# Kernel tuning notes

Measured on AMD Instinct MI355X. Metric: run time of the kernel, lower is better.

Reference implementation:

```python
import jax, jax.numpy as jnp
import numpy as np

B, M, L, D = 4, 128, 512, 768
NEG = -1e30


def setup_inputs() -> dict:
    key = jax.random.key(0)
    k1, k2 = jax.random.split(key)
    h = jax.random.normal(k1, (B, L, D), dtype=jnp.float32)
    mention_masks = jax.random.randint(k2, (B, M, L), 0, 2, dtype=jnp.int32)
    return {"h": h, "mention_masks": mention_masks}


def reference(h, mention_masks):
    # h: [B, L, D]; mention_masks: [B, M, L] (0/1)
    # Faithful to: m = (mask == 0).float() * -1e30; (m + h).max(dim=2)
    m = (mention_masks == 0).astype(h.dtype) * NEG          # [B, M, L]
    # broadcast add then max over token dim L -> [B, M, D]
    mention_reprs = jnp.max(h[:, None, :, :] + m[:, :, :, None], axis=2)
    return mention_reprs
```

## Files before the change

### kernel.cpp

```cpp
#include <hip/hip_runtime.h>

#define BB 4
#define MM 128
#define LL 512
#define DD 768
#define NEGF (-1e30f)

struct F3 { float x, y, z; };

__global__ __launch_bounds__(512, 2) void mention_max_kernel(
    const float* __restrict__ h, const int* __restrict__ mask,
    float* __restrict__ out)
{
    const int lane = threadIdx.x & 63;
    const int wave = threadIdx.x >> 6;
    const int dch  = blockIdx.x;
    const int mch  = blockIdx.y;
    const int b    = blockIdx.z;

    const int d0 = dch * 192 + lane * 3;
    const int m0 = mch * 8;
    const int l0 = wave * 64;

    const int* mp = mask + ((size_t)(b * MM + m0)) * LL + l0 + lane;
    int mv[8];
#pragma unroll
    for (int m = 0; m < 8; ++m) mv[m] = mp[m * LL];

    const F3* hp = (const F3*)(h + ((size_t)(b * LL + l0)) * DD + d0);
    F3 r0[32];
#pragma unroll
    for (int i = 0; i < 32; ++i) r0[i] = hp[(size_t)i * (DD / 3)];

    unsigned lobits[8], hibits[8];
#pragma unroll
    for (int m = 0; m < 8; ++m) {
        unsigned long long bl = __ballot(mv[m] != 0);
        lobits[m] = (unsigned)bl;
        hibits[m] = (unsigned)(bl >> 32);
    }

    F3 r1[32];
#pragma unroll
    for (int i = 0; i < 32; ++i) r1[i] = hp[(size_t)(i + 32) * (DD / 3)];

    F3 acc[8];
#pragma unroll
    for (int m = 0; m < 8; ++m) { acc[m].x = NEGF; acc[m].y = NEGF; acc[m].z = NEGF; }

#pragma unroll
    for (int m = 0; m < 8; ++m) {
        const unsigned w32 = lobits[m];
        F3 a = acc[m];
#pragma unroll
        for (int i = 0; i < 32; i += 2) {
            const float ad0 = ((w32 >> i) & 1u) ? 0.0f : NEGF;
            const float ad1 = ((w32 >> (i + 1)) & 1u) ? 0.0f : NEGF;
            a.x = fmaxf(fmaxf(r0[i].x + ad0, r0[i + 1].x + ad1), a.x);
            a.y = fmaxf(fmaxf(r0[i].y + ad0, r0[i + 1].y + ad1), a.y);
            a.z = fmaxf(fmaxf(r0[i].z + ad0, r0[i + 1].z + ad1), a.z);
        }
        acc[m] = a;
    }
#pragma unroll
    for (int m = 0; m < 8; ++m) {
        const unsigned w32 = hibits[m];
        F3 a = acc[m];
#pragma unroll
        for (int i = 0; i < 32; i += 2) {
            const float ad0 = ((w32 >> i) & 1u) ? 0.0f : NEGF;
            const float ad1 = ((w32 >> (i + 1)) & 1u) ? 0.0f : NEGF;
            a.x = fmaxf(fmaxf(r1[i].x + ad0, r1[i + 1].x + ad1), a.x);
            a.y = fmaxf(fmaxf(r1[i].y + ad0, r1[i + 1].y + ad1), a.y);
            a.z = fmaxf(fmaxf(r1[i].z + ad0, r1[i + 1].z + ad1), a.z);
        }
        acc[m] = a;
    }

    __shared__ float red[8][8][3][64];
#pragma unroll
    for (int m = 0; m < 8; ++m) {
        red[wave][m][0][lane] = acc[m].x;
        red[wave][m][1][lane] = acc[m].y;
        red[wave][m][2][lane] = acc[m].z;
    }
    __syncthreads();

    {
        const int m  = (int)(threadIdx.x >> 6);
        const int ln = (int)(threadIdx.x & 63);
        float vx = red[0][m][0][ln];
        float vy = red[0][m][1][ln];
        float vz = red[0][m][2][ln];
#pragma unroll
        for (int w = 1; w < 8; ++w) {
            vx = fmaxf(vx, red[w][m][0][ln]);
            vy = fmaxf(vy, red[w][m][1][ln]);
            vz = fmaxf(vz, red[w][m][2][ln]);
        }
        float* op = out + ((size_t)(b * MM + m0 + m)) * DD + dch * 192 + ln * 3;
        op[0] = vx;
        op[1] = vy;
        op[2] = vz;
    }
}

extern "C" void kernel_launch(void* const* d_in, const int* in_sizes, int n_in,
                              void* d_out, int out_size, void* d_ws, size_t ws_size,
                              hipStream_t stream) {
    const float* h    = (const float*)d_in[0];
    const int*   mask = (const int*)d_in[1];
    float*       out  = (float*)d_out;
    dim3 grid(DD / 192, MM / 8, BB);
    mention_max_kernel<<<grid, dim3(512), 0, stream>>>(h, mask, out);
}
```

Before: 73.01 us.

## Use 1024-thread blocks with smaller per-wave register tiles and software-pipelined loads

Each block now has 16 waves, each covering 32 tokens instead of 64. Every wave holds two 8-row register buffers that are double-buffered: the next batch of h rows loads while the current batch is reduced. Mask bits come from four ballots that pack two mention rows per wave. Cross-wave reduction gains a pairwise stage through shared memory. The aim is to cut register pressure and raise occupancy and latency hiding, at the cost of an extra barrier and more waves doing redundant mask loads.

```diff
diff --git a/kernel.cpp b/kernel.cpp
--- a/kernel.cpp
+++ b/kernel.cpp
@@ -8,7 +8,7 @@
 
 struct F3 { float x, y, z; };
 
-__global__ __launch_bounds__(512, 2) void mention_max_kernel(
+__global__ __launch_bounds__(1024, 4) void mention_max_kernel(
     const float* __restrict__ h, const int* __restrict__ mask,
     float* __restrict__ out)
 {
@@ -20,73 +20,86 @@
 
     const int d0 = dch * 192 + lane * 3;
     const int m0 = mch * 8;
-    const int l0 = wave * 64;
+    const int l0 = wave * 32;
 
-    const int* mp = mask + ((size_t)(b * MM + m0)) * LL + l0 + lane;
-    int mv[8];
-#pragma unroll
-    for (int m = 0; m < 8; ++m) mv[m] = mp[m * LL];
+    const int half = lane >> 5;
+    const int lrow = lane & 31;
+    const int* mp = mask + ((size_t)(b * MM + m0)) * LL + l0 + lrow;
+    int mv0 = mp[(0 + half) * LL];
+    int mv1 = mp[(2 + half) * LL];
+    int mv2 = mp[(4 + half) * LL];
+    int mv3 = mp[(6 + half) * LL];
 
     const F3* hp = (const F3*)(h + ((size_t)(b * LL + l0)) * DD + d0);
-    F3 r0[32];
+    F3 ra[8], rb[8];
 #pragma unroll
-    for (int i = 0; i < 32; ++i) r0[i] = hp[(size_t)i * (DD / 3)];
+    for (int i = 0; i < 8; ++i) ra[i] = hp[(size_t)i * (DD / 3)];
 
-    unsigned lobits[8], hibits[8];
+    unsigned wbits[8];
+    { unsigned long long bl = __ballot(mv0 != 0); wbits[0] = (unsigned)bl; wbits[1] = (unsigned)(bl >> 32); }
+    { unsigned long long bl = __ballot(mv1 != 0); wbits[2] = (unsigned)bl; wbits[3] = (unsigned)(bl >> 32); }
+    { unsigned long long bl = __ballot(mv2 != 0); wbits[4] = (unsigned)bl; wbits[5] = (unsigned)(bl >> 32); }
+    { unsigned long long bl = __ballot(mv3 != 0); wbits[6] = (unsigned)bl; wbits[7] = (unsigned)(bl >> 32); }
+
 #pragma unroll
-    for (int m = 0; m < 8; ++m) {
-        unsigned long long bl = __ballot(mv[m] != 0);
-        lobits[m] = (unsigned)bl;
-        hibits[m] = (unsigned)(bl >> 32);
-    }
-
-    F3 r1[32];
-#pragma unroll
-    for (int i = 0; i < 32; ++i) r1[i] = hp[(size_t)(i + 32) * (DD / 3)];
+    for (int i = 0; i < 8; ++i) rb[i] = hp[(size_t)(i + 8) * (DD / 3)];
 
     F3 acc[8];
 #pragma unroll
     for (int m = 0; m < 8; ++m) { acc[m].x = NEGF; acc[m].y = NEGF; acc[m].z = NEGF; }
 
+#define COMPUTE_BATCH(BUF, IB)                                                 \
+    do {                                                                       \
+        _Pragma("unroll")                                                      \
+        for (int m = 0; m < 8; ++m) {                                          \
+            const unsigned w32 = wbits[m] >> (IB);                             \
+            F3 a = acc[m];                                                     \
+            _Pragma("unroll")                                                  \
+            for (int i = 0; i < 8; i += 2) {                                   \
+                const float ad0 = ((w32 >> i) & 1u) ? 0.0f : NEGF;             \
+                const float ad1 = ((w32 >> (i + 1)) & 1u) ? 0.0f : NEGF;       \
+                a.x = fmaxf(fmaxf(BUF[i].x + ad0, BUF[i + 1].x + ad1), a.x);   \
+                a.y = fmaxf(fmaxf(BUF[i].y + ad0, BUF[i + 1].y + ad1), a.y);   \
+                a.z = fmaxf(fmaxf(BUF[i].z + ad0, BUF[i + 1].z + ad1), a.z);   \
+            }                                                                  \
+            acc[m] = a;                                                        \
+        }                                                                      \
+    } while (0)
+
+    COMPUTE_BATCH(ra, 0);
 #pragma unroll
-    for (int m = 0; m < 8; ++m) {
-        const unsigned w32 = lobits[m];
-        F3 a = acc[m];
+    for (int i = 0; i < 8; ++i) ra[i] = hp[(size_t)(i + 16) * (DD / 3)];
+    COMPUTE_BATCH(rb, 8);
 #pragma unroll
-        for (int i = 0; i < 32; i += 2) {
-            const float ad0 = ((w32 >> i) & 1u) ? 0.0f : NEGF;
-            const float ad1 = ((w32 >> (i + 1)) & 1u) ? 0.0f : NEGF;
-            a.x = fmaxf(fmaxf(r0[i].x + ad0, r0[i + 1].x + ad1), a.x);
-            a.y = fmaxf(fmaxf(r0[i].y + ad0, r0[i + 1].y + ad1), a.y);
-            a.z = fmaxf(fmaxf(r0[i].z + ad0, r0[i + 1].z + ad1), a.z);
-        }
-        acc[m] = a;
-    }
-#pragma unroll
-    for (int m = 0; m < 8; ++m) {
-        const unsigned w32 = hibits[m];
-        F3 a = acc[m];
-#pragma unroll
-        for (int i = 0; i < 32; i += 2) {
-            const float ad0 = ((w32 >> i) & 1u) ? 0.0f : NEGF;
-            const float ad1 = ((w32 >> (i + 1)) & 1u) ? 0.0f : NEGF;
-            a.x = fmaxf(fmaxf(r1[i].x + ad0, r1[i + 1].x + ad1), a.x);
-            a.y = fmaxf(fmaxf(r1[i].y + ad0, r1[i + 1].y + ad1), a.y);
-            a.z = fmaxf(fmaxf(r1[i].z + ad0, r1[i + 1].z + ad1), a.z);
-        }
-        acc[m] = a;
-    }
+    for (int i = 0; i < 8; ++i) rb[i] = hp[(size_t)(i + 24) * (DD / 3)];
+    COMPUTE_BATCH(ra, 16);
+    COMPUTE_BATCH(rb, 24);
+#undef COMPUTE_BATCH
 
     __shared__ float red[8][8][3][64];
+    if (wave >= 8) {
 #pragma unroll
-    for (int m = 0; m < 8; ++m) {
-        red[wave][m][0][lane] = acc[m].x;
-        red[wave][m][1][lane] = acc[m].y;
-        red[wave][m][2][lane] = acc[m].z;
+        for (int m = 0; m < 8; ++m) {
+            red[wave - 8][m][0][lane] = acc[m].x;
+            red[wave - 8][m][1][lane] = acc[m].y;
+            red[wave - 8][m][2][lane] = acc[m].z;
+        }
+    }
+    __syncthreads();
+    if (wave < 8) {
+#pragma unroll
+        for (int m = 0; m < 8; ++m) {
+            float vx = fmaxf(acc[m].x, red[wave][m][0][lane]);
+            float vy = fmaxf(acc[m].y, red[wave][m][1][lane]);
+            float vz = fmaxf(acc[m].z, red[wave][m][2][lane]);
+            red[wave][m][0][lane] = vx;
+            red[wave][m][1][lane] = vy;
+            red[wave][m][2][lane] = vz;
+        }
     }
     __syncthreads();
 
-    {
+    if (threadIdx.x < 512) {
         const int m  = (int)(threadIdx.x >> 6);
         const int ln = (int)(threadIdx.x & 63);
         float vx = red[0][m][0][ln];
@@ -112,5 +125,5 @@
     const int*   mask = (const int*)d_in[1];
     float*       out  = (float*)d_out;
     dim3 grid(DD / 192, MM / 8, BB);
-    mention_max_kernel<<<grid, dim3(512), 0, stream>>>(h, mask, out);
+    mention_max_kernel<<<grid, dim3(1024), 0, stream>>>(h, mask, out);
 }
```

New measurement: 68.67 us. -6.0%, faster.
